# Optimization experiments

Hardware: AMD Instinct MI355X
Metric: run time of the kernel (lower is better)

Reference implementation:

```python
import jax, jax.numpy as jnp
import numpy as np

D_MODEL = 1024
NUM_HEADS = 16
HEAD_DIM = D_MODEL // NUM_HEADS
THETA = 10000.0
BATCH, SEQ = 2, 2048


def rope(x, token_positions):
    # x: [b, h, s, d]; token_positions: [s]
    d = x.shape[-1]
    freqs = 1.0 / THETA ** (jnp.arange(0, d, 2, dtype=jnp.float32)[: d // 2] / d)
    ang = token_positions.astype(jnp.float32)[:, None] * freqs[None, :]  # [s, d/2]
    cos, sin = jnp.cos(ang), jnp.sin(ang)
    xr = x.reshape(*x.shape[:-1], d // 2, 2)
    x_even, x_odd = xr[..., 0], xr[..., 1]
    out_even = x_even * cos - x_odd * sin
    out_odd = x_even * sin + x_odd * cos
    return jnp.stack([out_even, out_odd], axis=-1).reshape(x.shape)


def setup_inputs() -> dict:
    key = jax.random.key(0)
    ks = jax.random.split(key, 5)
    std = np.sqrt(2.0 / (D_MODEL + D_MODEL))
    mk = lambda k: (jax.random.truncated_normal(k, -3.0, 3.0, (D_MODEL, D_MODEL), jnp.float32) * std)
    return {
        "x": jax.random.normal(ks[0], (BATCH, SEQ, D_MODEL), jnp.float32),
        "Wq": mk(ks[1]),
        "Wk": mk(ks[2]),
        "Wv": mk(ks[3]),
        "Wo": mk(ks[4]),
        "casual_mask": jnp.tril(jnp.ones((SEQ, SEQ), dtype=bool)),
        "token_positions": jnp.arange(SEQ, dtype=jnp.int32),
    }


def reference(x, Wq, Wk, Wv, Wo, casual_mask, token_positions):
    b, s, _ = x.shape
    split = lambda t: t.reshape(b, s, NUM_HEADS, HEAD_DIM).transpose(0, 2, 1, 3)
    q = split(x @ Wq.T)  # [b, h, s, d]
    k = split(x @ Wk.T)
    v = split(x @ Wv.T)
    q = rope(q, token_positions)
    k = rope(k, token_positions)
    scores = jnp.einsum("bhqd,bhkd->bhqk", q, k) / np.sqrt(HEAD_DIM)
    scores = jnp.where(casual_mask, scores, -jnp.inf)
    probs = jax.nn.softmax(scores, axis=-1)
    out = jnp.einsum("bhqk,bhkd->bhqd", probs, v)
    out = out.transpose(0, 2, 1, 3).reshape(b, s, D_MODEL)
    return out @ Wo.T
```

## Files before the change

### kernel.cpp

```cpp
#include <hip/hip_runtime.h>
#include <hip/hip_bf16.h>

#define SEQ_LEN 2048
#define NBATCH 2
#define DM 1024
#define NH 16
#define HD 64
#define NR (NBATCH * SEQ_LEN)
#define NQKV (3 * DM)
#define LDQK 2048

typedef __attribute__((ext_vector_type(8))) short bf16x8;
typedef __attribute__((ext_vector_type(4))) float f32x4;

__device__ __forceinline__ short f2b(float f) {
    __hip_bfloat16 h = __float2bfloat16(f);
    return *reinterpret_cast<short*>(&h);
}
__device__ __forceinline__ float b2f(short s) {
    union { unsigned u; float f; } x;
    x.u = ((unsigned)(unsigned short)s) << 16;
    return x.f;
}

__device__ __forceinline__ void gload_lds16(const void* g, void* l) {
    __builtin_amdgcn_global_load_lds(
        (const __attribute__((address_space(1))) unsigned int*)g,
        (__attribute__((address_space(3))) unsigned int*)l, 16, 0, 0);
}

__global__ __launch_bounds__(256) void cvt_all(
    const float* __restrict__ x,  const float* __restrict__ wq,
    const float* __restrict__ wk, const float* __restrict__ wv,
    const float* __restrict__ wo,
    __hip_bfloat16* __restrict__ xb, __hip_bfloat16* __restrict__ wqkvb,
    __hip_bfloat16* __restrict__ wob) {
    int id = blockIdx.x;
    const float* src; __hip_bfloat16* dst;
    if (id < 4096) { src = x + (size_t)id * 1024; dst = xb + (size_t)id * 1024; }
    else {
        int k = id - 4096, seg = k >> 10;
        size_t off = (size_t)(k & 1023) * 1024;
        if      (seg == 0) { src = wq + off; dst = wqkvb + off; }
        else if (seg == 1) { src = wk + off; dst = wqkvb + (1u << 20) + off; }
        else if (seg == 2) { src = wv + off; dst = wqkvb + (2u << 20) + off; }
        else               { src = wo + off; dst = wob + off; }
    }
    int i = threadIdx.x * 4;
    float4 v = *(const float4*)(src + i);
    dst[i + 0] = __float2bfloat16(v.x);
    dst[i + 1] = __float2bfloat16(v.y);
    dst[i + 2] = __float2bfloat16(v.z);
    dst[i + 3] = __float2bfloat16(v.w);
}

__device__ __forceinline__ void store_c(float* p, float v) { *p = v; }
__device__ __forceinline__ void store_c(__hip_bfloat16* p, float v) {
    *p = __float2bfloat16(v);
}

template <typename CT, bool FUSED>
__global__ __launch_bounds__(256) void gemm128(
    const __hip_bfloat16* __restrict__ A,
    const __hip_bfloat16* __restrict__ B,
    CT* __restrict__ C, int K, int ldc,
    __hip_bfloat16* __restrict__ Vtg, const int* __restrict__ pos) {
    __shared__ __hip_bfloat16 As[128 * 32];
    __shared__ __hip_bfloat16 Bs[128 * 32];
    const int t    = threadIdx.x;
    const int wave = t >> 6;
    const int lane = t & 63;
    const int quad = lane >> 4;
    const int l16  = lane & 15;
    const int wy = wave >> 1, wx = wave & 1;
    const int m0 = blockIdx.x * 128, n0 = blockIdx.y * 128;

    const int r0 = wave * 32 + (lane >> 2);
    const int c0 = (lane & 3) * 8;
    const __hip_bfloat16* Ag0 = A + (size_t)(m0 + r0) * K + c0;
    const __hip_bfloat16* Ag1 = Ag0 + (size_t)16 * K;
    const __hip_bfloat16* Bg0 = B + (size_t)(n0 + r0) * K + c0;
    const __hip_bfloat16* Bg1 = Bg0 + (size_t)16 * K;
    __hip_bfloat16* lA0 = &As[r0 * 32 + c0];
    __hip_bfloat16* lA1 = &As[(r0 + 16) * 32 + c0];
    __hip_bfloat16* lB0 = &Bs[r0 * 32 + c0];
    __hip_bfloat16* lB1 = &Bs[(r0 + 16) * 32 + c0];

    f32x4 acc[4][4];
#pragma unroll
    for (int i = 0; i < 4; i++)
#pragma unroll
        for (int j = 0; j < 4; j++) acc[i][j] = (f32x4){0.f, 0.f, 0.f, 0.f};

    for (int k0 = 0; k0 < K; k0 += 32) {
        __syncthreads();
        gload_lds16(Ag0 + k0, lA0);
        gload_lds16(Ag1 + k0, lA1);
        gload_lds16(Bg0 + k0, lB0);
        gload_lds16(Bg1 + k0, lB1);
        __syncthreads();

        bf16x8 af[4], bfr[4];
#pragma unroll
        for (int rb = 0; rb < 4; rb++)
            af[rb] = *(const bf16x8*)&As[(wy * 64 + rb * 16 + l16) * 32 + quad * 8];
#pragma unroll
        for (int cb = 0; cb < 4; cb++)
            bfr[cb] = *(const bf16x8*)&Bs[(wx * 64 + cb * 16 + l16) * 32 + quad * 8];
#pragma unroll
        for (int rb = 0; rb < 4; rb++)
#pragma unroll
            for (int cb = 0; cb < 4; cb++)
                acc[rb][cb] = __builtin_amdgcn_mfma_f32_16x16x32_bf16(
                    af[rb], bfr[cb], acc[rb][cb], 0, 0, 0);
    }

    if (!FUSED || blockIdx.y < 16) {
        if constexpr (FUSED) {
            const float sc = (blockIdx.y < 8) ? 0.125f : 1.0f;
            float fr[4];
#pragma unroll
            for (int cb = 0; cb < 4; cb++) {
                int i = ((cb * 16 + l16) & 63) >> 1;
                fr[cb] = __expf(-(float)(2 * i) * (9.210340371976184f / 64.0f));
            }
            const float par = (l16 & 1) ? 1.f : -1.f;
#pragma unroll
            for (int rb = 0; rb < 4; rb++)
#pragma unroll
                for (int r = 0; r < 4; r++) {
                    int row = m0 + wy * 64 + rb * 16 + quad * 4 + r;
                    float p = (float)pos[row & (SEQ_LEN - 1)];
#pragma unroll
                    for (int cb = 0; cb < 4; cb++) {
                        float sn, cs;
                        __sincosf(p * fr[cb], &sn, &cs);
                        float v  = acc[rb][cb][r];
                        float pt = __shfl_xor(v, 1);
                        acc[rb][cb][r] = (v * cs + par * pt * sn) * sc;
                    }
                }
        }
#pragma unroll
        for (int rb = 0; rb < 4; rb++)
#pragma unroll
            for (int r = 0; r < 4; r++) {
                size_t ro = (size_t)(m0 + wy * 64 + rb * 16 + quad * 4 + r) * ldc;
#pragma unroll
                for (int cb = 0; cb < 4; cb++)
                    store_c(&C[ro + n0 + wx * 64 + cb * 16 + l16], acc[rb][cb][r]);
            }
    } else {
#pragma unroll
        for (int rb = 0; rb < 4; rb++) {
            int row0 = m0 + wy * 64 + rb * 16 + quad * 4;
            int bb = row0 >> 11, ss = row0 & (SEQ_LEN - 1);
#pragma unroll
            for (int cb = 0; cb < 4; cb++) {
                int vcol = n0 + wx * 64 + cb * 16 + l16 - 2048;
                int hh = vcol >> 6, dd = vcol & 63;
                ushort4 u;
                u.x = (unsigned short)f2b(acc[rb][cb][0]);
                u.y = (unsigned short)f2b(acc[rb][cb][1]);
                u.z = (unsigned short)f2b(acc[rb][cb][2]);
                u.w = (unsigned short)f2b(acc[rb][cb][3]);
                *(ushort4*)(Vtg + ((size_t)(bb * NH + hh) * HD + dd) * SEQ_LEN + ss) = u;
            }
        }
    }
}

__global__ __launch_bounds__(256) void attn_kernel(
    const __hip_bfloat16* __restrict__ QK,
    const __hip_bfloat16* __restrict__ Vtg,
    __hip_bfloat16* __restrict__ O) {
    __shared__ __hip_bfloat16 Ks[2][64 * 64];
    __shared__ __hip_bfloat16 Vs[2][64 * 64];
    __shared__ short Ps[64][72];

    const int t    = threadIdx.x;
    const int wave = t >> 6;
    const int lane = t & 63;
    const int quad = lane >> 4;
    const int l16  = lane & 15;
    const int id  = blockIdx.x;
    const int qt  = 31 - (id >> 5);
    const int hb  = id & 31;
    const int h   = hb & 15;
    const int b   = hb >> 4;

    const int row0 = qt * 64 + wave * 16;

    const int sr  = t >> 3;
    const int scs = (t & 7) ^ (sr & 7);

    const __hip_bfloat16* kbase = QK + (size_t)(b * SEQ_LEN) * LDQK + DM + h * HD;
    const __hip_bfloat16* vbase = Vtg + (size_t)((b * NH + h) * HD) * SEQ_LEN;

#define STAGE(BUF, KT)                                                          \
    {                                                                           \
        gload_lds16(kbase + (size_t)((KT) * 64 + sr) * LDQK + scs * 8,          \
                    (char*)&Ks[BUF][0] + t * 16);                               \
        gload_lds16(kbase + (size_t)((KT) * 64 + sr + 32) * LDQK + scs * 8,     \
                    (char*)&Ks[BUF][0] + (t + 256) * 16);                       \
        gload_lds16(vbase + (size_t)sr * SEQ_LEN + (KT) * 64 + scs * 8,         \
                    (char*)&Vs[BUF][0] + t * 16);                               \
        gload_lds16(vbase + (size_t)(sr + 32) * SEQ_LEN + (KT) * 64 + scs * 8,  \
                    (char*)&Vs[BUF][0] + (t + 256) * 16);                       \
    }

#define LDS_FRAG(BASE, RR, G)                                                   \
    (*(const bf16x8*)((const char*)(BASE) + (RR) * 128 + ((((G) ^ ((RR) & 7))) << 4)))

#define TRIP(BUF, KT)                                                           \
    {                                                                           \
        bf16x8 kf[4][2];                                                        \
        _Pragma("unroll") for (int kb = 0; kb < 4; kb++) {                      \
            int rr = kb * 16 + l16;                                             \
            kf[kb][0] = LDS_FRAG(Ks[BUF], rr, quad);                            \
            kf[kb][1] = LDS_FRAG(Ks[BUF], rr, quad + 4);                        \
        }                                                                       \
        f32x4 s[4];                                                             \
        __builtin_amdgcn_s_setprio(1);                                          \
        _Pragma("unroll") for (int kb = 0; kb < 4; kb++) {                      \
            f32x4 z = {0.f, 0.f, 0.f, 0.f};                                     \
            z = __builtin_amdgcn_mfma_f32_16x16x32_bf16(qf0, kf[kb][0], z, 0, 0, 0); \
            z = __builtin_amdgcn_mfma_f32_16x16x32_bf16(qf1, kf[kb][1], z, 0, 0, 0); \
            s[kb] = z;                                                          \
        }                                                                       \
        __builtin_amdgcn_s_setprio(0);                                          \
        if ((KT) == qt) {                 \
            _Pragma("unroll") for (int kb = 0; kb < 4; kb++) {                  \
                int key = (KT) * 64 + kb * 16 + l16;                            \
                _Pragma("unroll") for (int r = 0; r < 4; r++) {                 \
                    int rowg = row0 + quad * 4 + r;                             \
                    if (key > rowg) s[kb][r] = -1e30f;                          \
                }                                                               \
            }                                                                   \
        }                                                                       \
        _Pragma("unroll") for (int r = 0; r < 4; r++) {                         \
            float p0 = __expf(s[0][r]);                                         \
            float p1 = __expf(s[1][r]);                                         \
            float p2 = __expf(s[2][r]);                                         \
            float p3 = __expf(s[3][r]);                                         \
            l_p[r] += (p0 + p1) + (p2 + p3);                                    \
            int prow = wave * 16 + quad * 4 + r;                                \
            Ps[prow][ 0 + l16] = f2b(p0);                                       \
            Ps[prow][16 + l16] = f2b(p1);                                       \
            Ps[prow][32 + l16] = f2b(p2);                                       \
            Ps[prow][48 + l16] = f2b(p3);                                       \
        }                                                                       \
        bf16x8 pf0 = *(const bf16x8*)&Ps[wave * 16 + l16][quad * 8];            \
        bf16x8 pf1 = *(const bf16x8*)&Ps[wave * 16 + l16][32 + quad * 8];       \
        __builtin_amdgcn_s_setprio(1);                                          \
        _Pragma("unroll") for (int db = 0; db < 4; db++) {                      \
            int rr = db * 16 + l16;                                             \
            bf16x8 vf0 = LDS_FRAG(Vs[BUF], rr, quad);                           \
            bf16x8 vf1 = LDS_FRAG(Vs[BUF], rr, quad + 4);                       \
            o[db] = __builtin_amdgcn_mfma_f32_16x16x32_bf16(pf0, vf0, o[db], 0, 0, 0); \
            o[db] = __builtin_amdgcn_mfma_f32_16x16x32_bf16(pf1, vf1, o[db], 0, 0, 0); \
        }                                                                       \
        __builtin_amdgcn_s_setprio(0);                                          \
    }

    bf16x8 qf0, qf1;
    {
        const __hip_bfloat16* qp =
            QK + (size_t)(b * SEQ_LEN + row0 + l16) * LDQK + h * HD + quad * 8;
        qf0 = *(const bf16x8*)qp;
        qf1 = *(const bf16x8*)(qp + 32);
    }
    f32x4 o[4];
    float l_p[4];
#pragma unroll
    for (int r = 0; r < 4; r++) { o[r] = (f32x4){0.f, 0.f, 0.f, 0.f}; l_p[r] = 0.f; }

    STAGE(0, 0);
    for (int kt = 0; kt <= qt; ++kt) {
        const int buf = kt & 1;
        __syncthreads();
        if (kt < qt) STAGE(buf ^ 1, kt + 1);
        TRIP(buf, kt);
    }

#pragma unroll
    for (int r = 0; r < 4; r++) {
        float rs = l_p[r];
        rs += __shfl_xor(rs, 1);
        rs += __shfl_xor(rs, 2);
        rs += __shfl_xor(rs, 4);
        rs += __shfl_xor(rs, 8);
        float inv = 1.0f / rs;
        size_t ro = (size_t)(b * SEQ_LEN + row0 + quad * 4 + r) * DM + h * HD;
        O[ro +  0 + l16] = __float2bfloat16(o[0][r] * inv);
        O[ro + 16 + l16] = __float2bfloat16(o[1][r] * inv);
        O[ro + 32 + l16] = __float2bfloat16(o[2][r] * inv);
        O[ro + 48 + l16] = __float2bfloat16(o[3][r] * inv);
    }
#undef STAGE
#undef LDS_FRAG
#undef TRIP
}

extern "C" void kernel_launch(void* const* d_in, const int* in_sizes, int n_in,
                              void* d_out, int out_size, void* d_ws, size_t ws_size,
                              hipStream_t stream) {
    const float* x  = (const float*)d_in[0];
    const float* Wq = (const float*)d_in[1];
    const float* Wk = (const float*)d_in[2];
    const float* Wv = (const float*)d_in[3];
    const float* Wo = (const float*)d_in[4];
    const int* pos = (const int*)d_in[6];
    float* out = (float*)d_out;

    char* w = (char*)d_ws;
    const size_t MiB = 1024 * 1024;
    __hip_bfloat16* xb    = (__hip_bfloat16*)(w + 0 * MiB);
    __hip_bfloat16* Ab    = (__hip_bfloat16*)(w + 0 * MiB);
    __hip_bfloat16* Wqkvb = (__hip_bfloat16*)(w + 8 * MiB);
    __hip_bfloat16* Wob   = (__hip_bfloat16*)(w + 14 * MiB);
    __hip_bfloat16* QKb   = (__hip_bfloat16*)(w + 16 * MiB);
    __hip_bfloat16* Vtg   = (__hip_bfloat16*)(w + 32 * MiB);

    cvt_all<<<8192, 256, 0, stream>>>(x, Wq, Wk, Wv, Wo, xb, Wqkvb, Wob);

    gemm128<__hip_bfloat16, true><<<dim3(NR / 128, NQKV / 128), 256, 0, stream>>>(
        xb, Wqkvb, QKb, DM, LDQK, Vtg, pos);

    attn_kernel<<<1024, 256, 0, stream>>>(QKb, Vtg, Ab);

    gemm128<float, false><<<dim3(NR / 128, DM / 128), 256, 0, stream>>>(
        Ab, Wob, out, DM, DM, nullptr, nullptr);
}
```

Before: 198.6 us.

## Use 32x32 MFMA in attention with register P, deepen GEMM K tile

The attention kernel is rewritten to compute S transposed with 32x32x16 MFMAs, so the exponentiated probabilities stay in registers and feed the PV MFMA directly. This removes the LDS round trip for P and its extra synchronisation. Each block now covers 128 query rows, with tiles ordered to balance causal work, and the V transpose store is permuted to match the new fragment layout. The GEMM K step doubles to 64 with an XOR-swizzled LDS layout, which halves barrier count but uses more LDS and registers.

```diff
diff --git a/kernel.cpp b/kernel.cpp
--- a/kernel.cpp
+++ b/kernel.cpp
@@ -12,15 +12,11 @@
 
 typedef __attribute__((ext_vector_type(8))) short bf16x8;
 typedef __attribute__((ext_vector_type(4))) float f32x4;
+typedef __attribute__((ext_vector_type(16))) float f32x16;
 
 __device__ __forceinline__ short f2b(float f) {
     __hip_bfloat16 h = __float2bfloat16(f);
     return *reinterpret_cast<short*>(&h);
-}
-__device__ __forceinline__ float b2f(short s) {
-    union { unsigned u; float f; } x;
-    x.u = ((unsigned)(unsigned short)s) << 16;
-    return x.f;
 }
 
 __device__ __forceinline__ void gload_lds16(const void* g, void* l) {
@@ -65,8 +61,8 @@
     const __hip_bfloat16* __restrict__ B,
     CT* __restrict__ C, int K, int ldc,
     __hip_bfloat16* __restrict__ Vtg, const int* __restrict__ pos) {
-    __shared__ __hip_bfloat16 As[128 * 32];
-    __shared__ __hip_bfloat16 Bs[128 * 32];
+    __shared__ __hip_bfloat16 As[128 * 64];
+    __shared__ __hip_bfloat16 Bs[128 * 64];
     const int t    = threadIdx.x;
     const int wave = t >> 6;
     const int lane = t & 63;
@@ -75,16 +71,11 @@
     const int wy = wave >> 1, wx = wave & 1;
     const int m0 = blockIdx.x * 128, n0 = blockIdx.y * 128;
 
-    const int r0 = wave * 32 + (lane >> 2);
-    const int c0 = (lane & 3) * 8;
-    const __hip_bfloat16* Ag0 = A + (size_t)(m0 + r0) * K + c0;
-    const __hip_bfloat16* Ag1 = Ag0 + (size_t)16 * K;
-    const __hip_bfloat16* Bg0 = B + (size_t)(n0 + r0) * K + c0;
-    const __hip_bfloat16* Bg1 = Bg0 + (size_t)16 * K;
-    __hip_bfloat16* lA0 = &As[r0 * 32 + c0];
-    __hip_bfloat16* lA1 = &As[(r0 + 16) * 32 + c0];
-    __hip_bfloat16* lB0 = &Bs[r0 * 32 + c0];
-    __hip_bfloat16* lB1 = &Bs[(r0 + 16) * 32 + c0];
+    const int sr  = t >> 3;
+    const int scx = (t & 7) ^ (sr & 7);
+
+    const __hip_bfloat16* Ag = A + (size_t)(m0 + sr) * K + scx * 8;
+    const __hip_bfloat16* Bg = B + (size_t)(n0 + sr) * K + scx * 8;
 
     f32x4 acc[4][4];
 #pragma unroll
@@ -92,27 +83,36 @@
 #pragma unroll
         for (int j = 0; j < 4; j++) acc[i][j] = (f32x4){0.f, 0.f, 0.f, 0.f};
 
-    for (int k0 = 0; k0 < K; k0 += 32) {
+    for (int k0 = 0; k0 < K; k0 += 64) {
         __syncthreads();
-        gload_lds16(Ag0 + k0, lA0);
-        gload_lds16(Ag1 + k0, lA1);
-        gload_lds16(Bg0 + k0, lB0);
-        gload_lds16(Bg1 + k0, lB1);
+#pragma unroll
+        for (int i = 0; i < 4; i++) {
+            gload_lds16(Ag + (size_t)(i * 32) * K + k0, (char*)As + (t + i * 256) * 16);
+            gload_lds16(Bg + (size_t)(i * 32) * K + k0, (char*)Bs + (t + i * 256) * 16);
+        }
         __syncthreads();
-
-        bf16x8 af[4], bfr[4];
-#pragma unroll
-        for (int rb = 0; rb < 4; rb++)
-            af[rb] = *(const bf16x8*)&As[(wy * 64 + rb * 16 + l16) * 32 + quad * 8];
-#pragma unroll
-        for (int cb = 0; cb < 4; cb++)
-            bfr[cb] = *(const bf16x8*)&Bs[(wx * 64 + cb * 16 + l16) * 32 + quad * 8];
-#pragma unroll
-        for (int rb = 0; rb < 4; rb++)
-#pragma unroll
-            for (int cb = 0; cb < 4; cb++)
-                acc[rb][cb] = __builtin_amdgcn_mfma_f32_16x16x32_bf16(
-                    af[rb], bfr[cb], acc[rb][cb], 0, 0, 0);
+#pragma unroll
+        for (int kk = 0; kk < 2; kk++) {
+            bf16x8 af[4], bfr[4];
+#pragma unroll
+            for (int rb = 0; rb < 4; rb++) {
+                int row = wy * 64 + rb * 16 + l16;
+                af[rb] = *(const bf16x8*)((const char*)As + row * 128 +
+                                          (((kk * 4 + quad) ^ (row & 7)) << 4));
+            }
+#pragma unroll
+            for (int cb = 0; cb < 4; cb++) {
+                int row = wx * 64 + cb * 16 + l16;
+                bfr[cb] = *(const bf16x8*)((const char*)Bs + row * 128 +
+                                           (((kk * 4 + quad) ^ (row & 7)) << 4));
+            }
+#pragma unroll
+            for (int rb = 0; rb < 4; rb++)
+#pragma unroll
+                for (int cb = 0; cb < 4; cb++)
+                    acc[rb][cb] = __builtin_amdgcn_mfma_f32_16x16x32_bf16(
+                        af[rb], bfr[cb], acc[rb][cb], 0, 0, 0);
+        }
     }
 
     if (!FUSED || blockIdx.y < 16) {
@@ -155,6 +155,7 @@
         for (int rb = 0; rb < 4; rb++) {
             int row0 = m0 + wy * 64 + rb * 16 + quad * 4;
             int bb = row0 >> 11, ss = row0 & (SEQ_LEN - 1);
+            int ssw = (ss & ~12) | ((ss & 4) << 1) | ((ss & 8) >> 1);
 #pragma unroll
             for (int cb = 0; cb < 4; cb++) {
                 int vcol = n0 + wx * 64 + cb * 16 + l16 - 2048;
@@ -164,141 +165,137 @@
                 u.y = (unsigned short)f2b(acc[rb][cb][1]);
                 u.z = (unsigned short)f2b(acc[rb][cb][2]);
                 u.w = (unsigned short)f2b(acc[rb][cb][3]);
-                *(ushort4*)(Vtg + ((size_t)(bb * NH + hh) * HD + dd) * SEQ_LEN + ss) = u;
+                *(ushort4*)(Vtg + ((size_t)(bb * NH + hh) * HD + dd) * SEQ_LEN + ssw) = u;
             }
         }
     }
 }
 
-__global__ __launch_bounds__(256) void attn_kernel(
+__global__ __launch_bounds__(256, 2) void attn_kernel(
     const __hip_bfloat16* __restrict__ QK,
     const __hip_bfloat16* __restrict__ Vtg,
     __hip_bfloat16* __restrict__ O) {
     __shared__ __hip_bfloat16 Ks[2][64 * 64];
     __shared__ __hip_bfloat16 Vs[2][64 * 64];
-    __shared__ short Ps[64][72];
 
     const int t    = threadIdx.x;
     const int wave = t >> 6;
     const int lane = t & 63;
-    const int quad = lane >> 4;
-    const int l16  = lane & 15;
-    const int id  = blockIdx.x;
-    const int qt  = 31 - (id >> 5);
-    const int hb  = id & 31;
-    const int h   = hb & 15;
-    const int b   = hb >> 4;
-
-    const int row0 = qt * 64 + wave * 16;
+    const int l5   = lane & 31;
+    const int hi   = lane >> 5;
+    const int id   = blockIdx.x;
+    const int qtc  = id >> 5;
+    const int hb   = id & 31;
+    const int h    = hb & 15;
+    const int b    = hb >> 4;
+    const int qt   = (qtc < 8) ? (15 - qtc) : (qtc - 8);
+
+    const int row0 = qt * 128 + wave * 32;
+    const int ktd  = (row0 + 31) >> 6;
+    const int KTM  = 2 * qt + 1;
 
     const int sr  = t >> 3;
-    const int scs = (t & 7) ^ (sr & 7);
+    const int scx = (t & 7) ^ (sr & 7);
 
     const __hip_bfloat16* kbase = QK + (size_t)(b * SEQ_LEN) * LDQK + DM + h * HD;
     const __hip_bfloat16* vbase = Vtg + (size_t)((b * NH + h) * HD) * SEQ_LEN;
 
+    bf16x8 qf[4];
+    {
+        const __hip_bfloat16* qp =
+            QK + (size_t)(b * SEQ_LEN + row0 + l5) * LDQK + h * HD + hi * 8;
+#pragma unroll
+        for (int dc = 0; dc < 4; dc++) qf[dc] = *(const bf16x8*)(qp + dc * 16);
+    }
+
+    f32x16 o0, o1;
+#pragma unroll
+    for (int i = 0; i < 16; i++) { o0[i] = 0.f; o1[i] = 0.f; }
+    float l_acc = 0.f;
+
 #define STAGE(BUF, KT)                                                          \
     {                                                                           \
-        gload_lds16(kbase + (size_t)((KT) * 64 + sr) * LDQK + scs * 8,          \
+        gload_lds16(kbase + (size_t)((KT) * 64 + sr) * LDQK + scx * 8,          \
                     (char*)&Ks[BUF][0] + t * 16);                               \
-        gload_lds16(kbase + (size_t)((KT) * 64 + sr + 32) * LDQK + scs * 8,     \
+        gload_lds16(kbase + (size_t)((KT) * 64 + sr + 32) * LDQK + scx * 8,     \
                     (char*)&Ks[BUF][0] + (t + 256) * 16);                       \
-        gload_lds16(vbase + (size_t)sr * SEQ_LEN + (KT) * 64 + scs * 8,         \
+        gload_lds16(vbase + (size_t)sr * SEQ_LEN + (KT) * 64 + scx * 8,         \
                     (char*)&Vs[BUF][0] + t * 16);                               \
-        gload_lds16(vbase + (size_t)(sr + 32) * SEQ_LEN + (KT) * 64 + scs * 8,  \
+        gload_lds16(vbase + (size_t)(sr + 32) * SEQ_LEN + (KT) * 64 + scx * 8,  \
                     (char*)&Vs[BUF][0] + (t + 256) * 16);                       \
     }
 
-#define LDS_FRAG(BASE, RR, G)                                                   \
-    (*(const bf16x8*)((const char*)(BASE) + (RR) * 128 + ((((G) ^ ((RR) & 7))) << 4)))
+#define LFRAG(BASE, ROW, CH)                                                    \
+    (*(const bf16x8*)((const char*)(BASE) + (ROW) * 128 + ((((CH) ^ ((ROW) & 7))) << 4)))
+
+#define MKPA(S, PA0, PA1)                                                       \
+    {                                                                           \
+        float p_[16];                                                           \
+        _Pragma("unroll") for (int r = 0; r < 16; r++) {                        \
+            p_[r] = __expf((S)[r]);                                             \
+            l_acc += p_[r];                                                     \
+        }                                                                       \
+        _Pragma("unroll") for (int j = 0; j < 8; j++) {                         \
+            PA0[j] = f2b(p_[j]);                                                \
+            PA1[j] = f2b(p_[8 + j]);                                            \
+        }                                                                       \
+    }
 
 #define TRIP(BUF, KT)                                                           \
     {                                                                           \
-        bf16x8 kf[4][2];                                                        \
-        _Pragma("unroll") for (int kb = 0; kb < 4; kb++) {                      \
-            int rr = kb * 16 + l16;                                             \
-            kf[kb][0] = LDS_FRAG(Ks[BUF], rr, quad);                            \
-            kf[kb][1] = LDS_FRAG(Ks[BUF], rr, quad + 4);                        \
-        }                                                                       \
-        f32x4 s[4];                                                             \
+        f32x16 s0, s1;                                                          \
+        _Pragma("unroll") for (int i = 0; i < 16; i++) { s0[i] = 0.f; s1[i] = 0.f; } \
         __builtin_amdgcn_s_setprio(1);                                          \
-        _Pragma("unroll") for (int kb = 0; kb < 4; kb++) {                      \
-            f32x4 z = {0.f, 0.f, 0.f, 0.f};                                     \
-            z = __builtin_amdgcn_mfma_f32_16x16x32_bf16(qf0, kf[kb][0], z, 0, 0, 0); \
-            z = __builtin_amdgcn_mfma_f32_16x16x32_bf16(qf1, kf[kb][1], z, 0, 0, 0); \
-            s[kb] = z;                                                          \
+        _Pragma("unroll") for (int dc = 0; dc < 4; dc++) {                      \
+            bf16x8 k0f = LFRAG(Ks[BUF], l5, dc * 2 + hi);                       \
+            bf16x8 k1f = LFRAG(Ks[BUF], 32 + l5, dc * 2 + hi);                  \
+            s0 = __builtin_amdgcn_mfma_f32_32x32x16_bf16(k0f, qf[dc], s0, 0, 0, 0); \
+            s1 = __builtin_amdgcn_mfma_f32_32x32x16_bf16(k1f, qf[dc], s1, 0, 0, 0); \
         }                                                                       \
         __builtin_amdgcn_s_setprio(0);                                          \
-        if ((KT) == qt) {                 \
-            _Pragma("unroll") for (int kb = 0; kb < 4; kb++) {                  \
-                int key = (KT) * 64 + kb * 16 + l16;                            \
-                _Pragma("unroll") for (int r = 0; r < 4; r++) {                 \
-                    int rowg = row0 + quad * 4 + r;                             \
-                    if (key > rowg) s[kb][r] = -1e30f;                          \
-                }                                                               \
+        if ((KT) == ktd) {                \
+            int qrow = row0 + l5;                                               \
+            _Pragma("unroll") for (int r = 0; r < 16; r++) {                    \
+                int key = (KT) * 64 + (r & 3) + 8 * (r >> 2) + 4 * hi;          \
+                if (key > qrow) s0[r] = -1e30f;                                 \
+                if (key + 32 > qrow) s1[r] = -1e30f;                            \
             }                                                                   \
         }                                                                       \
-        _Pragma("unroll") for (int r = 0; r < 4; r++) {                         \
-            float p0 = __expf(s[0][r]);                                         \
-            float p1 = __expf(s[1][r]);                                         \
-            float p2 = __expf(s[2][r]);                                         \
-            float p3 = __expf(s[3][r]);                                         \
-            l_p[r] += (p0 + p1) + (p2 + p3);                                    \
-            int prow = wave * 16 + quad * 4 + r;                                \
-            Ps[prow][ 0 + l16] = f2b(p0);                                       \
-            Ps[prow][16 + l16] = f2b(p1);                                       \
-            Ps[prow][32 + l16] = f2b(p2);                                       \
-            Ps[prow][48 + l16] = f2b(p3);                                       \
-        }                                                                       \
-        bf16x8 pf0 = *(const bf16x8*)&Ps[wave * 16 + l16][quad * 8];            \
-        bf16x8 pf1 = *(const bf16x8*)&Ps[wave * 16 + l16][32 + quad * 8];       \
+        bf16x8 pa0, pa1, pa2, pa3;                                              \
+        MKPA(s0, pa0, pa1);                                                     \
+        MKPA(s1, pa2, pa3);                                                     \
         __builtin_amdgcn_s_setprio(1);                                          \
-        _Pragma("unroll") for (int db = 0; db < 4; db++) {                      \
-            int rr = db * 16 + l16;                                             \
-            bf16x8 vf0 = LDS_FRAG(Vs[BUF], rr, quad);                           \
-            bf16x8 vf1 = LDS_FRAG(Vs[BUF], rr, quad + 4);                       \
-            o[db] = __builtin_amdgcn_mfma_f32_16x16x32_bf16(pf0, vf0, o[db], 0, 0, 0); \
-            o[db] = __builtin_amdgcn_mfma_f32_16x16x32_bf16(pf1, vf1, o[db], 0, 0, 0); \
+        _Pragma("unroll") for (int kc = 0; kc < 4; kc++) {                      \
+            bf16x8 v0f = LFRAG(Vs[BUF], l5, kc * 2 + hi);                       \
+            bf16x8 v1f = LFRAG(Vs[BUF], 32 + l5, kc * 2 + hi);                  \
+            bf16x8 paf = (kc == 0) ? pa0 : (kc == 1) ? pa1 : (kc == 2) ? pa2 : pa3; \
+            o0 = __builtin_amdgcn_mfma_f32_32x32x16_bf16(paf, v0f, o0, 0, 0, 0); \
+            o1 = __builtin_amdgcn_mfma_f32_32x32x16_bf16(paf, v1f, o1, 0, 0, 0); \
         }                                                                       \
         __builtin_amdgcn_s_setprio(0);                                          \
     }
 
-    bf16x8 qf0, qf1;
-    {
-        const __hip_bfloat16* qp =
-            QK + (size_t)(b * SEQ_LEN + row0 + l16) * LDQK + h * HD + quad * 8;
-        qf0 = *(const bf16x8*)qp;
-        qf1 = *(const bf16x8*)(qp + 32);
-    }
-    f32x4 o[4];
-    float l_p[4];
-#pragma unroll
-    for (int r = 0; r < 4; r++) { o[r] = (f32x4){0.f, 0.f, 0.f, 0.f}; l_p[r] = 0.f; }
-
     STAGE(0, 0);
-    for (int kt = 0; kt <= qt; ++kt) {
+    for (int kt = 0; kt <= KTM; ++kt) {
         const int buf = kt & 1;
         __syncthreads();
-        if (kt < qt) STAGE(buf ^ 1, kt + 1);
-        TRIP(buf, kt);
-    }
-
-#pragma unroll
-    for (int r = 0; r < 4; r++) {
-        float rs = l_p[r];
-        rs += __shfl_xor(rs, 1);
-        rs += __shfl_xor(rs, 2);
-        rs += __shfl_xor(rs, 4);
-        rs += __shfl_xor(rs, 8);
-        float inv = 1.0f / rs;
-        size_t ro = (size_t)(b * SEQ_LEN + row0 + quad * 4 + r) * DM + h * HD;
-        O[ro +  0 + l16] = __float2bfloat16(o[0][r] * inv);
-        O[ro + 16 + l16] = __float2bfloat16(o[1][r] * inv);
-        O[ro + 32 + l16] = __float2bfloat16(o[2][r] * inv);
-        O[ro + 48 + l16] = __float2bfloat16(o[3][r] * inv);
+        if (kt < KTM) STAGE(buf ^ 1, kt + 1);
+        if (kt <= ktd) TRIP(buf, kt);
+    }
+
+    l_acc += __shfl_xor(l_acc, 32);
+    float inv = 1.0f / l_acc;
+#pragma unroll
+    for (int r = 0; r < 16; r++) {
+        int crow  = (r & 3) + 8 * (r >> 2) + 4 * hi;
+        float invr = __shfl(inv, crow);
+        size_t ro = (size_t)(b * SEQ_LEN + row0 + crow) * DM + h * HD;
+        O[ro + l5]      = __float2bfloat16(o0[r] * invr);
+        O[ro + 32 + l5] = __float2bfloat16(o1[r] * invr);
     }
 #undef STAGE
-#undef LDS_FRAG
+#undef LFRAG
+#undef MKPA
 #undef TRIP
 }
 
@@ -327,7 +324,7 @@
     gemm128<__hip_bfloat16, true><<<dim3(NR / 128, NQKV / 128), 256, 0, stream>>>(
         xb, Wqkvb, QKb, DM, LDQK, Vtg, pos);
 
-    attn_kernel<<<1024, 256, 0, stream>>>(QKb, Vtg, Ab);
+    attn_kernel<<<512, 256, 0, stream>>>(QKb, Vtg, Ab);
 
     gemm128<float, false><<<dim3(NR / 128, DM / 128), 256, 0, stream>>>(
         Ab, Wob, out, DM, DM, nullptr, nullptr);
```

Measured after the change: 200.9 us. No clear change (+1.1%).
